# Kernel tuning notes

Measured on AMD Instinct MI355X. Metric: run time of the kernel, lower is better.

## Reference

```python
import jax, jax.numpy as jnp
import numpy as np

DROPOUT_P = 0.5
NUM_NODES = 50000


def _gcn_layer(x, W, b, src, dst, ew, num_nodes):
    # support = x @ W ; out = A_hat @ support + b, with A_hat given as edge list
    h = x @ W                               # [N, out_dim]
    msg = h[src] * ew[:, None]              # [E, out_dim]
    agg = jax.ops.segment_sum(msg, dst, num_segments=num_nodes)  # [N, out_dim]
    return agg + b


def setup_inputs() -> dict:
    key = jax.random.key(0)
    ks = jax.random.split(key, 8)
    N, E, F_in, H, C = NUM_NODES, 800000, 512, 128, 64
    x = jax.random.normal(ks[0], (N, F_in), dtype=jnp.float32)
    edge_weight = jax.random.uniform(ks[1], (E,), dtype=jnp.float32)
    W1 = jax.random.normal(ks[2], (F_in, H), dtype=jnp.float32) * (1.0 / np.sqrt(F_in))
    b1 = jax.random.normal(ks[3], (H,), dtype=jnp.float32) * 0.01
    W2 = jax.random.normal(ks[4], (H, C), dtype=jnp.float32) * (1.0 / np.sqrt(H))
    b2 = jax.random.normal(ks[5], (C,), dtype=jnp.float32) * 0.01
    drop_mask = jax.random.uniform(ks[6], (N, H), dtype=jnp.float32)
    edge_index = jax.random.randint(ks[7], (2, E), 0, N, dtype=jnp.int32)
    return {"x": x, "edge_weight": edge_weight, "W1": W1, "b1": b1,
            "W2": W2, "b2": b2, "drop_mask": drop_mask, "edge_index": edge_index}


def reference(x, edge_weight, W1, b1, W2, b2, drop_mask, edge_index):
    src, dst = edge_index[0], edge_index[1]
    h = _gcn_layer(x, W1, b1, src, dst, edge_weight, NUM_NODES)
    h = jax.nn.relu(h)
    # deterministic inverted dropout using precomputed uniform mask
    keep = (drop_mask >= DROPOUT_P).astype(h.dtype)
    h = h * keep / (1.0 - DROPOUT_P)
    h = _gcn_layer(h, W2, b2, src, dst, edge_weight, NUM_NODES)
    return jax.nn.log_softmax(h, axis=1)
```

## Files before the change

kernel.cpp:

```cpp
#include <hip/hip_runtime.h>
#include <cstdint>
#include <cstddef>

constexpr int FIN = 512;
constexpr int HD  = 128;
constexpr int CD  = 64;

typedef __attribute__((ext_vector_type(8))) short short8;
typedef __attribute__((ext_vector_type(4))) float f32x4;

__device__ inline unsigned short f2bf(float f) {
  unsigned int u = __float_as_uint(f);
  u += 0x7fffu + ((u >> 16) & 1u);
  return (unsigned short)(u >> 16);
}
__device__ inline float bf_lo(unsigned int v) { return __uint_as_float(v << 16); }
__device__ inline float bf_hi(unsigned int v) { return __uint_as_float(v & 0xffff0000u); }
__device__ inline float bf1(unsigned short v) { return __uint_as_float((unsigned int)v << 16); }


__global__ __launch_bounds__(256) void prep(const float* __restrict__ W1,
                                            const float* __restrict__ W2,
                                            unsigned short* __restrict__ w1t,
                                            unsigned short* __restrict__ w2t,
                                            int* __restrict__ cnt, int n) {
  int idx = blockIdx.x * 256 + threadIdx.x;
  if (idx < FIN * HD) {
    int k = idx >> 7, c = idx & 127;
    w1t[(size_t)c * FIN + k] = f2bf(W1[idx]);
  } else if (idx < FIN * HD + HD * CD) {
    int j = idx - FIN * HD;
    int k = j >> 6, c = j & 63;
    w2t[(size_t)c * HD + k] = f2bf(W2[j]);
  }
  if (idx < n) cnt[idx] = 0;
}


__global__ __launch_bounds__(256) void scan_a(const int* __restrict__ cnt,
                                              int* __restrict__ bs, int n) {
  __shared__ int sh[256];
  int t = threadIdx.x;
  int base = blockIdx.x * 2048;
  int s = 0;
#pragma unroll
  for (int j = 0; j < 8; ++j) {
    int idx = base + j * 256 + t;
    if (idx < n) s += cnt[idx];
  }
  sh[t] = s;
  __syncthreads();
  for (int o = 128; o > 0; o >>= 1) {
    if (t < o) sh[t] += sh[t + o];
    __syncthreads();
  }
  if (t == 0) bs[blockIdx.x] = sh[0];
}

__global__ __launch_bounds__(256) void scan_c(const int* __restrict__ cnt,
                                              const int* __restrict__ bs,
                                              int* __restrict__ off,
                                              int* __restrict__ cur, int n) {
  __shared__ int sh[256];
  __shared__ int sbase;
  const int t   = threadIdx.x;
  const int bid = blockIdx.x;
  if (t < 64) {
    int v = (t < bid) ? bs[t] : 0;
#pragma unroll
    for (int o = 32; o > 0; o >>= 1) v += __shfl_xor(v, o, 64);
    if (t == 0) sbase = v;
  }
  const int base = bid * 2048 + t * 8;
  int v[8];
  int local = 0;
#pragma unroll
  for (int j = 0; j < 8; ++j) {
    v[j] = (base + j < n) ? cnt[base + j] : 0;
    local += v[j];
  }
  sh[t] = local;
  __syncthreads();
  for (int o = 1; o < 256; o <<= 1) {
    int u = (t >= o) ? sh[t - o] : 0;
    __syncthreads();
    sh[t] += u;
    __syncthreads();
  }
  int run = sbase + sh[t] - local;
#pragma unroll
  for (int j = 0; j < 8; ++j) {
    if (base + j < n) { off[base + j] = run; cur[base + j] = run; }
    run += v[j];
  }
}


__global__ __launch_bounds__(256) void scatter_kernel(const int* __restrict__ src,
                                                      const int* __restrict__ dst,
                                                      const float* __restrict__ ew, int E,
                                                      int* __restrict__ cur,
                                                      int2* __restrict__ sew) {
  int i = blockIdx.x * 256 + threadIdx.x;
  if (i < E) {
    int d = dst[i];
    int p = atomicAdd(&cur[d], 1);
    sew[p] = make_int2(src[i], __float_as_int(ew[i]));
  }
}


__global__ __launch_bounds__(256) void gemm1_mfma(const float* __restrict__ x,
                                                  const unsigned short* __restrict__ w1t,
                                                  unsigned short* __restrict__ h1b, int M,
                                                  const int* __restrict__ dst, int E,
                                                  int* __restrict__ cnt) {
  {
    const int stride = gridDim.x * 256;
    for (int i = blockIdx.x * 256 + threadIdx.x; i < E; i += stride)
      atomicAdd(&cnt[dst[i]], 1);
  }

  __shared__ unsigned short As[64][72];
  __shared__ unsigned short Bs[128][72];
  const int t    = threadIdx.x;
  const int wave = t >> 6;
  const int lane = t & 63;
  const int l15  = lane & 15;
  const int quad = lane >> 4;
  const int m0   = blockIdx.x * 64;

  const int ar = t >> 2;
  const int ak = (t & 3) * 16;
  const int br = t >> 1;
  const int bk = (t & 1) * 32;

  const bool aok = (m0 + ar) < M;
  const float* xrow = x + (size_t)(m0 + ar) * FIN + ak;
  const unsigned short* brow = w1t + (size_t)br * FIN + bk;

  f32x4 acc[8];
#pragma unroll
  for (int j = 0; j < 8; ++j) acc[j] = (f32x4)0.f;

  for (int k0 = 0; k0 < FIN; k0 += 64) {
    float4 a0 = make_float4(0.f, 0.f, 0.f, 0.f), a1 = a0, a2 = a0, a3 = a0;
    if (aok) {
      a0 = *(const float4*)(xrow + k0);
      a1 = *(const float4*)(xrow + k0 + 4);
      a2 = *(const float4*)(xrow + k0 + 8);
      a3 = *(const float4*)(xrow + k0 + 12);
    }
    uint4 b0 = *(const uint4*)(brow + k0);
    uint4 b1 = *(const uint4*)(brow + k0 + 8);
    uint4 b2 = *(const uint4*)(brow + k0 + 16);
    uint4 b3 = *(const uint4*)(brow + k0 + 24);
    __syncthreads();
    unsigned short tmp[16];
    tmp[0]  = f2bf(a0.x); tmp[1]  = f2bf(a0.y); tmp[2]  = f2bf(a0.z); tmp[3]  = f2bf(a0.w);
    tmp[4]  = f2bf(a1.x); tmp[5]  = f2bf(a1.y); tmp[6]  = f2bf(a1.z); tmp[7]  = f2bf(a1.w);
    tmp[8]  = f2bf(a2.x); tmp[9]  = f2bf(a2.y); tmp[10] = f2bf(a2.z); tmp[11] = f2bf(a2.w);
    tmp[12] = f2bf(a3.x); tmp[13] = f2bf(a3.y); tmp[14] = f2bf(a3.z); tmp[15] = f2bf(a3.w);
    *(uint4*)&As[ar][ak]     = ((const uint4*)tmp)[0];
    *(uint4*)&As[ar][ak + 8] = ((const uint4*)tmp)[1];
    *(uint4*)&Bs[br][bk]      = b0;
    *(uint4*)&Bs[br][bk + 8]  = b1;
    *(uint4*)&Bs[br][bk + 16] = b2;
    *(uint4*)&Bs[br][bk + 24] = b3;
    __syncthreads();
#pragma unroll
    for (int ks = 0; ks < 64; ks += 32) {
      short8 af = *(const short8*)&As[wave * 16 + l15][ks + quad * 8];
#pragma unroll
      for (int nt = 0; nt < 8; ++nt) {
        short8 bf = *(const short8*)&Bs[nt * 16 + l15][ks + quad * 8];
        acc[nt] = __builtin_amdgcn_mfma_f32_16x16x32_bf16(af, bf, acc[nt], 0, 0, 0);
      }
    }
  }
  const int row0 = m0 + wave * 16 + quad * 4;
#pragma unroll
  for (int r = 0; r < 4; ++r) {
    int row = row0 + r;
    if (row < M) {
      unsigned short* orow = h1b + (size_t)row * HD + l15;
#pragma unroll
      for (int nt = 0; nt < 8; ++nt) orow[nt * 16] = f2bf(acc[nt][r]);
    }
  }
}


__global__ __launch_bounds__(256) void agg1_kernel(const unsigned int* __restrict__ h1b,
                                                   const float* __restrict__ b1,
                                                   const float* __restrict__ dm,
                                                   const int* __restrict__ off,
                                                   const int* __restrict__ cnt,
                                                   const int2* __restrict__ sew,
                                                   unsigned int* __restrict__ hbf, int N) {
  const int wave = threadIdx.x >> 6;
  const int lane = threadIdx.x & 63;
  const int node = blockIdx.x * 4 + wave;
  if (node >= N) return;
  const int start = off[node];
  const int deg   = cnt[node];
  const int2* ep  = sew + start;

  float a0 = 0.f, a1 = 0.f, c0 = 0.f, c1 = 0.f;
  float e0 = 0.f, e1 = 0.f, g0 = 0.f, g1 = 0.f;
  int e = 0;
  for (; e + 8 <= deg; e += 8) {
    int2 p0 = ep[e + 0], p1 = ep[e + 1], p2 = ep[e + 2], p3 = ep[e + 3];
    int2 p4 = ep[e + 4], p5 = ep[e + 5], p6 = ep[e + 6], p7 = ep[e + 7];
    unsigned int v0 = h1b[(size_t)p0.x * 64 + lane];
    unsigned int v1 = h1b[(size_t)p1.x * 64 + lane];
    unsigned int v2 = h1b[(size_t)p2.x * 64 + lane];
    unsigned int v3 = h1b[(size_t)p3.x * 64 + lane];
    unsigned int v4 = h1b[(size_t)p4.x * 64 + lane];
    unsigned int v5 = h1b[(size_t)p5.x * 64 + lane];
    unsigned int v6 = h1b[(size_t)p6.x * 64 + lane];
    unsigned int v7 = h1b[(size_t)p7.x * 64 + lane];
    float w0 = __int_as_float(p0.y), w1 = __int_as_float(p1.y);
    float w2 = __int_as_float(p2.y), w3 = __int_as_float(p3.y);
    float w4 = __int_as_float(p4.y), w5 = __int_as_float(p5.y);
    float w6 = __int_as_float(p6.y), w7 = __int_as_float(p7.y);
    a0 = fmaf(bf_lo(v0), w0, a0); a1 = fmaf(bf_hi(v0), w0, a1);
    c0 = fmaf(bf_lo(v1), w1, c0); c1 = fmaf(bf_hi(v1), w1, c1);
    e0 = fmaf(bf_lo(v2), w2, e0); e1 = fmaf(bf_hi(v2), w2, e1);
    g0 = fmaf(bf_lo(v3), w3, g0); g1 = fmaf(bf_hi(v3), w3, g1);
    a0 = fmaf(bf_lo(v4), w4, a0); a1 = fmaf(bf_hi(v4), w4, a1);
    c0 = fmaf(bf_lo(v5), w5, c0); c1 = fmaf(bf_hi(v5), w5, c1);
    e0 = fmaf(bf_lo(v6), w6, e0); e1 = fmaf(bf_hi(v6), w6, e1);
    g0 = fmaf(bf_lo(v7), w7, g0); g1 = fmaf(bf_hi(v7), w7, g1);
  }
  for (; e + 4 <= deg; e += 4) {
    int2 p0 = ep[e + 0], p1 = ep[e + 1], p2 = ep[e + 2], p3 = ep[e + 3];
    unsigned int v0 = h1b[(size_t)p0.x * 64 + lane];
    unsigned int v1 = h1b[(size_t)p1.x * 64 + lane];
    unsigned int v2 = h1b[(size_t)p2.x * 64 + lane];
    unsigned int v3 = h1b[(size_t)p3.x * 64 + lane];
    float w0 = __int_as_float(p0.y), w1 = __int_as_float(p1.y);
    float w2 = __int_as_float(p2.y), w3 = __int_as_float(p3.y);
    a0 = fmaf(bf_lo(v0), w0, a0); a1 = fmaf(bf_hi(v0), w0, a1);
    c0 = fmaf(bf_lo(v1), w1, c0); c1 = fmaf(bf_hi(v1), w1, c1);
    e0 = fmaf(bf_lo(v2), w2, e0); e1 = fmaf(bf_hi(v2), w2, e1);
    g0 = fmaf(bf_lo(v3), w3, g0); g1 = fmaf(bf_hi(v3), w3, g1);
  }
  for (; e < deg; ++e) {
    int2 p = ep[e];
    unsigned int v = h1b[(size_t)p.x * 64 + lane];
    float w = __int_as_float(p.y);
    a0 = fmaf(bf_lo(v), w, a0); a1 = fmaf(bf_hi(v), w, a1);
  }
  a0 += c0 + e0 + g0; a1 += c1 + e1 + g1;

  const int f0 = lane * 2;
  float2 bb = *(const float2*)(b1 + f0);
  float2 dd = *(const float2*)(dm + (size_t)node * HD + f0);
  float r0 = fmaxf(a0 + bb.x, 0.f) * ((dd.x >= 0.5f) ? 2.0f : 0.0f);
  float r1 = fmaxf(a1 + bb.y, 0.f) * ((dd.y >= 0.5f) ? 2.0f : 0.0f);
  hbf[(size_t)node * 64 + lane] = (unsigned int)f2bf(r0) | ((unsigned int)f2bf(r1) << 16);
}


__global__ __launch_bounds__(256) void gemm2_mfma(const unsigned short* __restrict__ hbf,
                                                  const unsigned short* __restrict__ w2t,
                                                  unsigned short* __restrict__ h2b, int M) {
  __shared__ unsigned short As[128][40];
  __shared__ unsigned short Bs[64][40];
  const int t    = threadIdx.x;
  const int wave = t >> 6;
  const int lane = t & 63;
  const int l15  = lane & 15;
  const int quad = lane >> 4;
  const int m0   = blockIdx.x * 128;

  const int sr = t >> 1;
  const int sk = (t & 1) * 16;
  const int rb = t >> 2;
  const int kb = (t & 3) * 8;

  const bool aok = (m0 + sr) < M;
  const unsigned short* arow = hbf + (size_t)(m0 + sr) * HD + sk;
  const unsigned short* brow = w2t + (size_t)rb * HD + kb;

  f32x4 acc[2][4];
#pragma unroll
  for (int i = 0; i < 2; ++i)
#pragma unroll
    for (int j = 0; j < 4; ++j) acc[i][j] = (f32x4)0.f;

  for (int k0 = 0; k0 < HD; k0 += 32) {
    uint4 av0 = make_uint4(0, 0, 0, 0), av1 = av0;
    if (aok) {
      av0 = *(const uint4*)(arow + k0);
      av1 = *(const uint4*)(arow + k0 + 8);
    }
    uint4 bv = *(const uint4*)(brow + k0);
    __syncthreads();
    *(uint4*)&As[sr][sk]     = av0;
    *(uint4*)&As[sr][sk + 8] = av1;
    *(uint4*)&Bs[rb][kb]     = bv;
    __syncthreads();
    short8 af0 = *(const short8*)&As[wave * 32 + l15][quad * 8];
    short8 af1 = *(const short8*)&As[wave * 32 + 16 + l15][quad * 8];
#pragma unroll
    for (int nt = 0; nt < 4; ++nt) {
      short8 bf = *(const short8*)&Bs[nt * 16 + l15][quad * 8];
      acc[0][nt] = __builtin_amdgcn_mfma_f32_16x16x32_bf16(af0, bf, acc[0][nt], 0, 0, 0);
      acc[1][nt] = __builtin_amdgcn_mfma_f32_16x16x32_bf16(af1, bf, acc[1][nt], 0, 0, 0);
    }
  }
#pragma unroll
  for (int mt = 0; mt < 2; ++mt) {
    const int row0 = m0 + wave * 32 + mt * 16 + quad * 4;
#pragma unroll
    for (int r = 0; r < 4; ++r) {
      int row = row0 + r;
      if (row < M) {
        unsigned short* orow = h2b + (size_t)row * CD + l15;
#pragma unroll
        for (int nt = 0; nt < 4; ++nt) orow[nt * 16] = f2bf(acc[mt][nt][r]);
      }
    }
  }
}


__global__ __launch_bounds__(256) void agg2_kernel(const unsigned short* __restrict__ h2b,
                                                   const float* __restrict__ b2,
                                                   const int* __restrict__ off,
                                                   const int* __restrict__ cnt,
                                                   const int2* __restrict__ sew,
                                                   float* __restrict__ out, int N) {
  const int wave = threadIdx.x >> 6;
  const int c    = threadIdx.x & 63;
  const int node = blockIdx.x * 4 + wave;
  if (node >= N) return;
  const int start = off[node];
  const int deg   = cnt[node];
  const int2* ep  = sew + start;

  float acc = b2[c], a1 = 0.f, a2 = 0.f, a3 = 0.f;
  int e = 0;
  for (; e + 8 <= deg; e += 8) {
    int2 p0 = ep[e + 0], p1 = ep[e + 1], p2 = ep[e + 2], p3 = ep[e + 3];
    int2 p4 = ep[e + 4], p5 = ep[e + 5], p6 = ep[e + 6], p7 = ep[e + 7];
    float v0 = bf1(h2b[(size_t)p0.x * CD + c]);
    float v1 = bf1(h2b[(size_t)p1.x * CD + c]);
    float v2 = bf1(h2b[(size_t)p2.x * CD + c]);
    float v3 = bf1(h2b[(size_t)p3.x * CD + c]);
    float v4 = bf1(h2b[(size_t)p4.x * CD + c]);
    float v5 = bf1(h2b[(size_t)p5.x * CD + c]);
    float v6 = bf1(h2b[(size_t)p6.x * CD + c]);
    float v7 = bf1(h2b[(size_t)p7.x * CD + c]);
    acc = fmaf(v0, __int_as_float(p0.y), acc);
    a1  = fmaf(v1, __int_as_float(p1.y), a1);
    a2  = fmaf(v2, __int_as_float(p2.y), a2);
    a3  = fmaf(v3, __int_as_float(p3.y), a3);
    acc = fmaf(v4, __int_as_float(p4.y), acc);
    a1  = fmaf(v5, __int_as_float(p5.y), a1);
    a2  = fmaf(v6, __int_as_float(p6.y), a2);
    a3  = fmaf(v7, __int_as_float(p7.y), a3);
  }
  for (; e + 4 <= deg; e += 4) {
    int2 p0 = ep[e + 0], p1 = ep[e + 1], p2 = ep[e + 2], p3 = ep[e + 3];
    float v0 = bf1(h2b[(size_t)p0.x * CD + c]);
    float v1 = bf1(h2b[(size_t)p1.x * CD + c]);
    float v2 = bf1(h2b[(size_t)p2.x * CD + c]);
    float v3 = bf1(h2b[(size_t)p3.x * CD + c]);
    acc = fmaf(v0, __int_as_float(p0.y), acc);
    a1  = fmaf(v1, __int_as_float(p1.y), a1);
    a2  = fmaf(v2, __int_as_float(p2.y), a2);
    a3  = fmaf(v3, __int_as_float(p3.y), a3);
  }
  for (; e < deg; ++e) {
    int2 p = ep[e];
    acc = fmaf(bf1(h2b[(size_t)p.x * CD + c]), __int_as_float(p.y), acc);
  }
  acc += a1 + a2 + a3;

  float m = acc;
#pragma unroll
  for (int o = 32; o > 0; o >>= 1) m = fmaxf(m, __shfl_xor(m, o, 64));
  float ex = __expf(acc - m);
  float ssum = ex;
#pragma unroll
  for (int o = 32; o > 0; o >>= 1) ssum += __shfl_xor(ssum, o, 64);
  out[(size_t)node * CD + c] = (acc - m) - __logf(ssum);
}


extern "C" void kernel_launch(void* const* d_in, const int* in_sizes, int n_in,
                              void* d_out, int out_size, void* d_ws, size_t ws_size,
                              hipStream_t stream) {
  const float* x  = (const float*)d_in[0];
  const float* ew = (const float*)d_in[1];
  const float* W1 = (const float*)d_in[2];
  const float* b1 = (const float*)d_in[3];
  const float* W2 = (const float*)d_in[4];
  const float* b2 = (const float*)d_in[5];
  const float* dm = (const float*)d_in[6];
  const int*   ei = (const int*)d_in[7];
  float* out = (float*)d_out;

  const int E = in_sizes[1];
  const int N = in_sizes[6] / HD;
  const int* srcp = ei;
  const int* dstp = ei + E;
  const int nb = (N + 2047) / 2048;

  uint8_t* w = (uint8_t*)d_ws;
  size_t o = 0;
  auto alloc = [&](size_t bytes) -> void* {
    void* p = w + o;
    o = (o + bytes + 255) & ~(size_t)255;
    return p;
  };
  int*   off    = (int*)alloc((size_t)N * 4);
  int*   cnt    = (int*)alloc((size_t)N * 4);
  int*   cur    = (int*)alloc((size_t)N * 4);
  int2*  sew    = (int2*)alloc((size_t)E * 8);
  unsigned short* h1b = (unsigned short*)alloc((size_t)N * HD * 2);
  unsigned int*   hbf = (unsigned int*)alloc((size_t)N * HD * 2);
  unsigned short* h2b = (unsigned short*)alloc((size_t)N * CD * 2);
  unsigned short* w1t = (unsigned short*)alloc((size_t)FIN * HD * 2);
  unsigned short* w2t = (unsigned short*)alloc((size_t)HD * CD * 2);
  int*   bsum   = (int*)alloc((size_t)nb * 4);

  const int prep_threads = FIN * HD + HD * CD;
  prep<<<(prep_threads + 255) / 256, 256, 0, stream>>>(W1, W2, w1t, w2t, cnt, N);
  gemm1_mfma<<<(N + 63) / 64, 256, 0, stream>>>(x, w1t, h1b, N, dstp, E, cnt);
  scan_a<<<nb, 256, 0, stream>>>(cnt, bsum, N);
  scan_c<<<nb, 256, 0, stream>>>(cnt, bsum, off, cur, N);
  scatter_kernel<<<(E + 255) / 256, 256, 0, stream>>>(srcp, dstp, ew, E, cur, sew);
  agg1_kernel<<<(N + 3) / 4, 256, 0, stream>>>((const unsigned int*)h1b, b1, dm, off, cnt, sew, hbf, N);
  gemm2_mfma<<<(N + 127) / 128, 256, 0, stream>>>((const unsigned short*)hbf, w2t, h2b, N);
  agg2_kernel<<<(N + 3) / 4, 256, 0, stream>>>(h2b, b2, off, cnt, sew, out, N);
}
```

Measured before the change: 361.2 us.

## Replicate degree counters to cut atomic contention and prefetch GEMM1 tiles

The in-degree histogram is split across 8 replicated count arrays indexed by block, so concurrent atomics land on different addresses. The scan kernels sum the replicas, and the result is stored in a new deg array that the aggregation kernels now read. Separately, the GEMM1 main loop is software-pipelined: the next K-tile's global loads are issued before the MFMA work on the current tile. This costs extra memory for the replicas, extra reads during the scan, a larger prep zeroing pass, and more registers in GEMM1.

```diff
diff --git a/kernel.cpp b/kernel.cpp
--- a/kernel.cpp
+++ b/kernel.cpp
@@ -5,6 +5,7 @@
 constexpr int FIN = 512;
 constexpr int HD  = 128;
 constexpr int CD  = 64;
+constexpr int NREP = 8;
 
 typedef __attribute__((ext_vector_type(8))) short short8;
 typedef __attribute__((ext_vector_type(4))) float f32x4;
@@ -23,7 +24,7 @@
                                             const float* __restrict__ W2,
                                             unsigned short* __restrict__ w1t,
                                             unsigned short* __restrict__ w2t,
-                                            int* __restrict__ cnt, int n) {
+                                            int* __restrict__ cnt, int n8) {
   int idx = blockIdx.x * 256 + threadIdx.x;
   if (idx < FIN * HD) {
     int k = idx >> 7, c = idx & 127;
@@ -33,7 +34,7 @@
     int k = j >> 6, c = j & 63;
     w2t[(size_t)c * HD + k] = f2bf(W2[j]);
   }
-  if (idx < n) cnt[idx] = 0;
+  if (idx < n8) cnt[idx] = 0;
 }
 
 
@@ -46,7 +47,10 @@
 #pragma unroll
   for (int j = 0; j < 8; ++j) {
     int idx = base + j * 256 + t;
-    if (idx < n) s += cnt[idx];
+    if (idx < n) {
+#pragma unroll
+      for (int r = 0; r < NREP; ++r) s += cnt[(size_t)r * n + idx];
+    }
   }
   sh[t] = s;
   __syncthreads();
@@ -60,7 +64,8 @@
 __global__ __launch_bounds__(256) void scan_c(const int* __restrict__ cnt,
                                               const int* __restrict__ bs,
                                               int* __restrict__ off,
-                                              int* __restrict__ cur, int n) {
+                                              int* __restrict__ cur,
+                                              int* __restrict__ deg, int n) {
   __shared__ int sh[256];
   __shared__ int sbase;
   const int t   = threadIdx.x;
@@ -76,8 +81,13 @@
   int local = 0;
 #pragma unroll
   for (int j = 0; j < 8; ++j) {
-    v[j] = (base + j < n) ? cnt[base + j] : 0;
-    local += v[j];
+    int s = 0;
+    if (base + j < n) {
+#pragma unroll
+      for (int r = 0; r < NREP; ++r) s += cnt[(size_t)r * n + base + j];
+    }
+    v[j] = s;
+    local += s;
   }
   sh[t] = local;
   __syncthreads();
@@ -90,7 +100,7 @@
   int run = sbase + sh[t] - local;
 #pragma unroll
   for (int j = 0; j < 8; ++j) {
-    if (base + j < n) { off[base + j] = run; cur[base + j] = run; }
+    if (base + j < n) { off[base + j] = run; cur[base + j] = run; deg[base + j] = v[j]; }
     run += v[j];
   }
 }
@@ -114,11 +124,12 @@
                                                   const unsigned short* __restrict__ w1t,
                                                   unsigned short* __restrict__ h1b, int M,
                                                   const int* __restrict__ dst, int E,
-                                                  int* __restrict__ cnt) {
+                                                  int* __restrict__ cnt, int Nn) {
   {
+    int* rep = cnt + (size_t)(blockIdx.x & (NREP - 1)) * Nn;
     const int stride = gridDim.x * 256;
     for (int i = blockIdx.x * 256 + threadIdx.x; i < E; i += stride)
-      atomicAdd(&cnt[dst[i]], 1);
+      atomicAdd(&rep[dst[i]], 1);
   }
 
   __shared__ unsigned short As[64][72];
@@ -143,31 +154,49 @@
 #pragma unroll
   for (int j = 0; j < 8; ++j) acc[j] = (f32x4)0.f;
 
+  float4 pa0 = make_float4(0.f, 0.f, 0.f, 0.f), pa1 = pa0, pa2 = pa0, pa3 = pa0;
+  if (aok) {
+    pa0 = *(const float4*)(xrow + 0);
+    pa1 = *(const float4*)(xrow + 4);
+    pa2 = *(const float4*)(xrow + 8);
+    pa3 = *(const float4*)(xrow + 12);
+  }
+  uint4 pb0 = *(const uint4*)(brow + 0);
+  uint4 pb1 = *(const uint4*)(brow + 8);
+  uint4 pb2 = *(const uint4*)(brow + 16);
+  uint4 pb3 = *(const uint4*)(brow + 24);
+
   for (int k0 = 0; k0 < FIN; k0 += 64) {
-    float4 a0 = make_float4(0.f, 0.f, 0.f, 0.f), a1 = a0, a2 = a0, a3 = a0;
-    if (aok) {
-      a0 = *(const float4*)(xrow + k0);
-      a1 = *(const float4*)(xrow + k0 + 4);
-      a2 = *(const float4*)(xrow + k0 + 8);
-      a3 = *(const float4*)(xrow + k0 + 12);
-    }
-    uint4 b0 = *(const uint4*)(brow + k0);
-    uint4 b1 = *(const uint4*)(brow + k0 + 8);
-    uint4 b2 = *(const uint4*)(brow + k0 + 16);
-    uint4 b3 = *(const uint4*)(brow + k0 + 24);
     __syncthreads();
     unsigned short tmp[16];
-    tmp[0]  = f2bf(a0.x); tmp[1]  = f2bf(a0.y); tmp[2]  = f2bf(a0.z); tmp[3]  = f2bf(a0.w);
-    tmp[4]  = f2bf(a1.x); tmp[5]  = f2bf(a1.y); tmp[6]  = f2bf(a1.z); tmp[7]  = f2bf(a1.w);
-    tmp[8]  = f2bf(a2.x); tmp[9]  = f2bf(a2.y); tmp[10] = f2bf(a2.z); tmp[11] = f2bf(a2.w);
-    tmp[12] = f2bf(a3.x); tmp[13] = f2bf(a3.y); tmp[14] = f2bf(a3.z); tmp[15] = f2bf(a3.w);
-    *(uint4*)&As[ar][ak]     = ((const uint4*)tmp)[0];
-    *(uint4*)&As[ar][ak + 8] = ((const uint4*)tmp)[1];
-    *(uint4*)&Bs[br][bk]      = b0;
-    *(uint4*)&Bs[br][bk + 8]  = b1;
-    *(uint4*)&Bs[br][bk + 16] = b2;
-    *(uint4*)&Bs[br][bk + 24] = b3;
-    __syncthreads();
+    tmp[0]  = f2bf(pa0.x); tmp[1]  = f2bf(pa0.y); tmp[2]  = f2bf(pa0.z); tmp[3]  = f2bf(pa0.w);
+    tmp[4]  = f2bf(pa1.x); tmp[5]  = f2bf(pa1.y); tmp[6]  = f2bf(pa1.z); tmp[7]  = f2bf(pa1.w);
+    tmp[8]  = f2bf(pa2.x); tmp[9]  = f2bf(pa2.y); tmp[10] = f2bf(pa2.z); tmp[11] = f2bf(pa2.w);
+    tmp[12] = f2bf(pa3.x); tmp[13] = f2bf(pa3.y); tmp[14] = f2bf(pa3.z); tmp[15] = f2bf(pa3.w);
+    *(uint4*)&As[ar][ak]      = ((const uint4*)tmp)[0];
+    *(uint4*)&As[ar][ak + 8]  = ((const uint4*)tmp)[1];
+    *(uint4*)&Bs[br][bk]      = pb0;
+    *(uint4*)&Bs[br][bk + 8]  = pb1;
+    *(uint4*)&Bs[br][bk + 16] = pb2;
+    *(uint4*)&Bs[br][bk + 24] = pb3;
+    __syncthreads();
+
+    const bool more = (k0 + 64) < FIN;
+    float4 qa0 = make_float4(0.f, 0.f, 0.f, 0.f), qa1 = qa0, qa2 = qa0, qa3 = qa0;
+    uint4 qb0 = make_uint4(0, 0, 0, 0), qb1 = qb0, qb2 = qb0, qb3 = qb0;
+    if (more) {
+      if (aok) {
+        qa0 = *(const float4*)(xrow + k0 + 64);
+        qa1 = *(const float4*)(xrow + k0 + 68);
+        qa2 = *(const float4*)(xrow + k0 + 72);
+        qa3 = *(const float4*)(xrow + k0 + 76);
+      }
+      qb0 = *(const uint4*)(brow + k0 + 64);
+      qb1 = *(const uint4*)(brow + k0 + 72);
+      qb2 = *(const uint4*)(brow + k0 + 80);
+      qb3 = *(const uint4*)(brow + k0 + 88);
+    }
+
 #pragma unroll
     for (int ks = 0; ks < 64; ks += 32) {
       short8 af = *(const short8*)&As[wave * 16 + l15][ks + quad * 8];
@@ -177,6 +206,8 @@
         acc[nt] = __builtin_amdgcn_mfma_f32_16x16x32_bf16(af, bf, acc[nt], 0, 0, 0);
       }
     }
+    pa0 = qa0; pa1 = qa1; pa2 = qa2; pa3 = qa3;
+    pb0 = qb0; pb1 = qb1; pb2 = qb2; pb3 = qb3;
   }
   const int row0 = m0 + wave * 16 + quad * 4;
 #pragma unroll
@@ -418,8 +449,9 @@
     return p;
   };
   int*   off    = (int*)alloc((size_t)N * 4);
-  int*   cnt    = (int*)alloc((size_t)N * 4);
+  int*   cnt    = (int*)alloc((size_t)NREP * N * 4);
   int*   cur    = (int*)alloc((size_t)N * 4);
+  int*   deg    = (int*)alloc((size_t)N * 4);
   int2*  sew    = (int2*)alloc((size_t)E * 8);
   unsigned short* h1b = (unsigned short*)alloc((size_t)N * HD * 2);
   unsigned int*   hbf = (unsigned int*)alloc((size_t)N * HD * 2);
@@ -428,13 +460,14 @@
   unsigned short* w2t = (unsigned short*)alloc((size_t)HD * CD * 2);
   int*   bsum   = (int*)alloc((size_t)nb * 4);
 
-  const int prep_threads = FIN * HD + HD * CD;
-  prep<<<(prep_threads + 255) / 256, 256, 0, stream>>>(W1, W2, w1t, w2t, cnt, N);
-  gemm1_mfma<<<(N + 63) / 64, 256, 0, stream>>>(x, w1t, h1b, N, dstp, E, cnt);
+  const int wcvt = FIN * HD + HD * CD;
+  const int prep_threads = (wcvt > NREP * N) ? wcvt : NREP * N;
+  prep<<<(prep_threads + 255) / 256, 256, 0, stream>>>(W1, W2, w1t, w2t, cnt, NREP * N);
+  gemm1_mfma<<<(N + 63) / 64, 256, 0, stream>>>(x, w1t, h1b, N, dstp, E, cnt, N);
   scan_a<<<nb, 256, 0, stream>>>(cnt, bsum, N);
-  scan_c<<<nb, 256, 0, stream>>>(cnt, bsum, off, cur, N);
+  scan_c<<<nb, 256, 0, stream>>>(cnt, bsum, off, cur, deg, N);
   scatter_kernel<<<(E + 255) / 256, 256, 0, stream>>>(srcp, dstp, ew, E, cur, sew);
-  agg1_kernel<<<(N + 3) / 4, 256, 0, stream>>>((const unsigned int*)h1b, b1, dm, off, cnt, sew, hbf, N);
+  agg1_kernel<<<(N + 3) / 4, 256, 0, stream>>>((const unsigned int*)h1b, b1, dm, off, deg, sew, hbf, N);
   gemm2_mfma<<<(N + 127) / 128, 256, 0, stream>>>((const unsigned short*)hbf, w2t, h2b, N);
-  agg2_kernel<<<(N + 3) / 4, 256, 0, stream>>>(h2b, b2, off, cnt, sew, out, N);
-}
+  agg2_kernel<<<(N + 3) / 4, 256, 0, stream>>>(h2b, b2, off, deg, sew, out, N);
+}
```

Result: no change. 361.2 us (-0.0%).
